# Kernel tuning notes

Measured on AMD Instinct MI355X. Metric: run time of the kernel, lower is better.

## Reference

```python
import jax, jax.numpy as jnp
import numpy as np

D_MODEL = 1024
NUM_HEADS = 16
HEAD_DIM = D_MODEL // NUM_HEADS
B, S = 2, 2048
EPS = 1e-8


def setup_inputs() -> dict:
    key = jax.random.key(0)
    ks = jax.random.split(key, 9)
    sc = 1.0 / np.sqrt(D_MODEL)
    return {
        "x": jax.random.normal(ks[0], (B, S, D_MODEL), jnp.float32),
        "wq": jax.random.normal(ks[1], (D_MODEL, D_MODEL), jnp.float32) * sc,
        "bq": jax.random.normal(ks[2], (D_MODEL,), jnp.float32) * 0.01,
        "wk": jax.random.normal(ks[3], (D_MODEL, D_MODEL), jnp.float32) * sc,
        "bk": jax.random.normal(ks[4], (D_MODEL,), jnp.float32) * 0.01,
        "wv": jax.random.normal(ks[5], (D_MODEL, D_MODEL), jnp.float32) * sc,
        "bv": jax.random.normal(ks[6], (D_MODEL,), jnp.float32) * 0.01,
        "wo": jax.random.normal(ks[7], (D_MODEL, D_MODEL), jnp.float32) * sc,
        "bo": jax.random.normal(ks[8], (D_MODEL,), jnp.float32) * 0.01,
    }


def reference(x, wq, bq, wk, bk, wv, bv, wo, bo):
    b, s, d = x.shape
    h, hd = NUM_HEADS, HEAD_DIM
    # projections (torch Linear: y = x W^T + b); reshape to [b, h, s, hd]
    def proj(w, bias):
        return (jnp.einsum('bsd,ed->bse', x, w) + bias).reshape(b, s, h, hd).transpose(0, 2, 1, 3)
    q = proj(wq, bq)
    k = proj(wk, bk)
    v = proj(wv, bv)
    scores = jnp.einsum('bhqd,bhkd->bhqk', q, k) / np.sqrt(hd)
    attn = jax.nn.softmax(scores, axis=-1)
    o = jnp.einsum('bhqk,bhkd->bhqd', attn, v)  # [b, h, s, hd]
    # per-position, per-head Gram-Schmidt exclusion: remove component of o[i]
    # along v[i] (the loop in the original is independent over positions)
    v_norm_sq = jnp.sum(v * v, axis=-1, keepdims=True)          # [b,h,s,1]
    align = jnp.sum(o * v, axis=-1, keepdims=True) / (v_norm_sq + EPS)
    o = o - align * v
    o = o.transpose(0, 2, 1, 3).reshape(b, s, d)
    return jnp.einsum('bsd,ed->bse', o, wo) + bo
```

## Files before the change

### kernel.cpp

```cpp
#include <hip/hip_runtime.h>
#include <stdint.h>

#define SEQ 2048
#define NTOK 4096
#define DM 1024

typedef __bf16 bf16x8 __attribute__((ext_vector_type(8)));
typedef __bf16 bf16x4 __attribute__((ext_vector_type(4)));
typedef float f32x4 __attribute__((ext_vector_type(4)));

__device__ __forceinline__ unsigned short f2bf(float f) {
  union { float f; unsigned u; } v; v.f = f;
  return (unsigned short)((v.u + 0x7fffu + ((v.u >> 16) & 1u)) >> 16);
}
__device__ __forceinline__ float bf2f(unsigned short s) {
  union { unsigned u; float f; } v; v.u = ((unsigned)s) << 16; return v.f;
}
__device__ __forceinline__ unsigned pkbf(float a, float b) {
  union { float f; unsigned u; } x, y; x.f = a; y.f = b;
  return __builtin_amdgcn_perm(y.u + 0x8000u, x.u + 0x8000u, 0x07060302u);
}

__device__ __forceinline__ void async16(const unsigned short* g, unsigned short* l) {
  __builtin_amdgcn_global_load_lds(
      (const __attribute__((address_space(1))) void*)g,
      (__attribute__((address_space(3))) void*)l, 16, 0, 0);
}

__global__ __launch_bounds__(256) void cast_all(
    const float* __restrict__ x, const float* __restrict__ wq,
    const float* __restrict__ wk, const float* __restrict__ wv,
    const float* __restrict__ wo, unsigned short* __restrict__ dst) {
  size_t i = ((size_t)blockIdx.x * 256 + threadIdx.x) * 4;
  const float* src; size_t off;
  if (i < (size_t)NTOK * DM) { src = x; off = i; }
  else {
    size_t j = i - (size_t)NTOK * DM;
    int s = (int)(j >> 20);
    src = (s == 0) ? wq : (s == 1) ? wk : (s == 2) ? wv : wo;
    off = j & 1048575u;
  }
  float4 f = *(const float4*)(src + off);
  ushort4 o;
  o.x = f2bf(f.x); o.y = f2bf(f.y); o.z = f2bf(f.z); o.w = f2bf(f.w);
  *(ushort4*)(dst + i) = o;
}

__device__ __forceinline__ void gemm128_bk64(
    const unsigned short* __restrict__ A, const unsigned short* __restrict__ Bw,
    int m0, int n0, f32x4 acc[4][4], unsigned short* As, unsigned short* Bs) {
  const int tid = threadIdx.x, lane = tid & 63, w = tid >> 6;
  const int wm = (w >> 1) * 64, wn = (w & 1) * 64;
  const int quad = lane >> 4, l16 = lane & 15, sel = l16 & 7;
  const int srow = tid >> 3;
  const int sc = ((tid & 7) ^ (srow & 7)) << 3;

  for (int kt = 0; kt < 1024; kt += 64) {
    __syncthreads();
#pragma unroll
    for (int c = 0; c < 4; ++c) {
      const int row = c * 32 + srow;
      async16(A + (size_t)(m0 + row) * 1024 + kt + sc, As + c * 2048 + tid * 8);
      async16(Bw + (size_t)(n0 + row) * 1024 + kt + sc, Bs + c * 2048 + tid * 8);
    }
    __syncthreads();
#pragma unroll
    for (int ks = 0; ks < 2; ++ks) {
      bf16x8 af[4], bf[4];
#pragma unroll
      for (int i = 0; i < 4; ++i)
        af[i] = *(const bf16x8*)(As + (wm + i * 16 + l16) * 64 + (((ks * 4 + quad) ^ sel) << 3));
#pragma unroll
      for (int j = 0; j < 4; ++j)
        bf[j] = *(const bf16x8*)(Bs + (wn + j * 16 + l16) * 64 + (((ks * 4 + quad) ^ sel) << 3));
#pragma unroll
      for (int i = 0; i < 4; ++i)
#pragma unroll
        for (int j = 0; j < 4; ++j)
          acc[i][j] = __builtin_amdgcn_mfma_f32_16x16x32_bf16(af[i], bf[j], acc[i][j], 0, 0, 0);
    }
  }
}

__global__ __launch_bounds__(256) void qkv_gemm(
    const unsigned short* __restrict__ xb,
    const unsigned short* __restrict__ wqb, const unsigned short* __restrict__ wkb,
    const unsigned short* __restrict__ wvb,
    const float* __restrict__ bq, const float* __restrict__ bk, const float* __restrict__ bv,
    unsigned short* __restrict__ Q, unsigned short* __restrict__ Kd,
    unsigned short* __restrict__ Vt) {
  __shared__ unsigned short As[128 * 64], Bs[128 * 64];
  const int kind = blockIdx.z;
  const unsigned short* A; const unsigned short* Bw;
  int m0, n0;
  if (kind == 2) { A = wvb; Bw = xb; m0 = blockIdx.x * 128; n0 = blockIdx.y * 128; }
  else { A = xb; Bw = (kind == 0) ? wqb : wkb; m0 = blockIdx.y * 128; n0 = blockIdx.x * 128; }
  f32x4 acc[4][4];
#pragma unroll
  for (int i = 0; i < 4; ++i)
#pragma unroll
    for (int j = 0; j < 4; ++j) { f32x4 z = {0.f, 0.f, 0.f, 0.f}; acc[i][j] = z; }
  gemm128_bk64(A, Bw, m0, n0, acc, As, Bs);

  const int lane = threadIdx.x & 63, w = threadIdx.x >> 6;
  const int quad = lane >> 4, l16 = lane & 15;
  const int wm = (w >> 1) * 64, wn = (w & 1) * 64;

  if (kind == 2) {
#pragma unroll
    for (int i = 0; i < 4; ++i)
#pragma unroll
      for (int j = 0; j < 4; ++j) {
        const int n = n0 + wn + j * 16 + l16;
        const int tb = n >> 11, s = n & 2047;
#pragma unroll
        for (int r = 0; r < 4; ++r) {
          const int m = m0 + wm + i * 16 + quad * 4 + r;
          const int h = m >> 6, d = m & 63;
          Vt[((size_t)(tb * 16 + h) * 64 + d) * SEQ + s] = f2bf(acc[i][j][r] + bv[m]);
        }
      }
  } else {
    const float* bias = (kind == 0) ? bq : bk;
    const float scale = (kind == 0) ? 0.180336880f : 1.0f;
#pragma unroll
    for (int i = 0; i < 4; ++i)
#pragma unroll
      for (int j = 0; j < 4; ++j) {
        const int col = n0 + wn + j * 16 + l16;
        const float bb = bias[col];
        const int h = col >> 6, d = col & 63;
#pragma unroll
        for (int r = 0; r < 4; ++r) {
          const int m = m0 + wm + i * 16 + quad * 4 + r;
          const int b = m >> 11, s = m & 2047;
          const int bh = b * 16 + h;
          const unsigned short val = f2bf((acc[i][j][r] + bb) * scale);
          if (kind == 0) Q[((size_t)bh * SEQ + s) * 64 + d] = val;
          else           Kd[((size_t)bh * SEQ + s) * 64 + d] = val;
        }
      }
  }
}

__global__ __launch_bounds__(256, 2) void attn_kernel(
    const unsigned short* __restrict__ Q, const unsigned short* __restrict__ Kd,
    const unsigned short* __restrict__ Vt,
    unsigned short* __restrict__ Op, float* __restrict__ Lp) {
  __shared__ unsigned short KV[4][4096];
  const int gx = blockIdx.x;
  const int xcd = gx & 7;
  const int idx = gx >> 3;
  const int bh  = xcd * 4 + (idx & 3);
  const int ksl = (idx >> 2) & 1;
  const int q0  = (idx >> 3) * 256;
  const int ks0 = ksl << 10;
  const int tid = threadIdx.x, lane = tid & 63, w = tid >> 6;
  const int quad = lane >> 4, l16 = lane & 15;
  const unsigned short* Qp = Q + (size_t)bh * SEQ * 64;
  const unsigned short* Kp = Kd + (size_t)bh * SEQ * 64;
  const unsigned short* Vp = Vt + (size_t)bh * 64 * SEQ;
  const int srow = tid >> 3;
  const int sc = ((tid & 7) ^ (srow & 7)) << 3;

#pragma unroll
  for (int c = 0; c < 8; ++c)
    async16(Qp + (size_t)(q0 + c * 32 + srow) * 64 + sc,
            KV[c >> 1] + (c & 1) * 2048 + tid * 8);
  __syncthreads();

  const int sel = l16 & 7;
  const unsigned short* Qsrc = KV[w];
  bf16x8 bQ[4][2];
#pragma unroll
  for (int qq = 0; qq < 4; ++qq) {
    const int qrow = qq * 16 + l16;
#pragma unroll
    for (int hh = 0; hh < 2; ++hh)
      bQ[qq][hh] = *(const bf16x8*)(Qsrc + qrow * 64 + (((hh * 4 + quad) ^ sel) << 3));
  }
  __syncthreads();

  async16(Kp + (size_t)(ks0 + srow) * 64 + sc, KV[0] + tid * 8);
  async16(Kp + (size_t)(ks0 + 32 + srow) * 64 + sc, KV[0] + 2048 + tid * 8);
  async16(Vp + (size_t)srow * SEQ + ks0 + sc, KV[2] + tid * 8);
  async16(Vp + (size_t)(32 + srow) * SEQ + ks0 + sc, KV[2] + 2048 + tid * 8);

  union { unsigned short u[8]; bf16x8 v; } one8;
#pragma unroll
  for (int t = 0; t < 8; ++t) one8.u[t] = 0x3F80;
  const bf16x8 aOnes = one8.v;

  f32x4 o_acc[4][4];
  f32x4 l_acc[4];
  const f32x4 zinit = {-12.f, -12.f, -12.f, -12.f};
#pragma unroll
  for (int qq = 0; qq < 4; ++qq) {
    f32x4 z = {0.f, 0.f, 0.f, 0.f};
    l_acc[qq] = z;
#pragma unroll
    for (int dt = 0; dt < 4; ++dt) o_acc[qq][dt] = z;
  }

  for (int it = 0; it < 16; ++it) {
    const int cur = it & 1;
    __syncthreads();
    if (it + 1 < 16) {
      const int kt = ks0 + (it + 1) * 64, nb = (it + 1) & 1;
      async16(Kp + (size_t)(kt + srow) * 64 + sc, KV[nb] + tid * 8);
      async16(Kp + (size_t)(kt + 32 + srow) * 64 + sc, KV[nb] + 2048 + tid * 8);
      async16(Vp + (size_t)srow * SEQ + kt + sc, KV[2 + nb] + tid * 8);
      async16(Vp + (size_t)(32 + srow) * SEQ + kt + sc, KV[2 + nb] + 2048 + tid * 8);
    }
    const unsigned short* Ks = KV[cur];
    const unsigned short* Vs = KV[2 + cur];

    bf16x8 bP[4][2];
#pragma unroll
    for (int kk = 0; kk < 4; ++kk) {
      const int krow = kk * 16 + l16;
      bf16x8 a0 = *(const bf16x8*)(Ks + krow * 64 + ((quad ^ sel) << 3));
      bf16x8 a1 = *(const bf16x8*)(Ks + krow * 64 + (((4 + quad) ^ sel) << 3));
#pragma unroll
      for (int qq = 0; qq < 4; ++qq) {
        f32x4 z = __builtin_amdgcn_mfma_f32_16x16x32_bf16(a0, bQ[qq][0], zinit, 0, 0, 0);
        z = __builtin_amdgcn_mfma_f32_16x16x32_bf16(a1, bQ[qq][1], z, 0, 0, 0);
#pragma unroll
        for (int r = 0; r < 4; ++r) z[r] = __builtin_amdgcn_exp2f(z[r]);
        unsigned lo = pkbf(z[0], z[1]);
        unsigned hi = pkbf(z[2], z[3]);
        union { unsigned d[4]; bf16x8 v; } pk;
        pk.v = bP[qq][kk >> 1];
        pk.d[(kk & 1) * 2] = lo;
        pk.d[(kk & 1) * 2 + 1] = hi;
        bP[qq][kk >> 1] = pk.v;
      }
    }

#pragma unroll
    for (int qq = 0; qq < 4; ++qq)
#pragma unroll
      for (int G = 0; G < 2; ++G)
        l_acc[qq] = __builtin_amdgcn_mfma_f32_16x16x32_bf16(aOnes, bP[qq][G], l_acc[qq], 0, 0, 0);

#pragma unroll
    for (int dt = 0; dt < 4; ++dt) {
      const unsigned short* vbase = Vs + (dt * 16 + l16) * 64;
      const int inner = (quad & 1) * 4;
#pragma unroll
      for (int G = 0; G < 2; ++G) {
        const int c0 = 4 * G + (quad >> 1);
        bf16x4 lo = *(const bf16x4*)(vbase + ((c0 ^ sel) << 3) + inner);
        bf16x4 hi = *(const bf16x4*)(vbase + (((c0 + 2) ^ sel) << 3) + inner);
        bf16x8 aV = __builtin_shufflevector(lo, hi, 0, 1, 2, 3, 4, 5, 6, 7);
#pragma unroll
        for (int qq = 0; qq < 4; ++qq)
          o_acc[qq][dt] = __builtin_amdgcn_mfma_f32_16x16x32_bf16(aV, bP[qq][G], o_acc[qq][dt], 0, 0, 0);
      }
    }
  }

  const size_t sb = (size_t)(ksl * 32 + bh);
#pragma unroll
  for (int qq = 0; qq < 4; ++qq) {
    const int qg = q0 + w * 64 + qq * 16 + l16;
#pragma unroll
    for (int dt = 0; dt < 4; ++dt)
#pragma unroll
      for (int r = 0; r < 4; ++r) {
        const int d = dt * 16 + quad * 4 + r;
        Op[(sb * 64 + d) * SEQ + qg] = f2bf(o_acc[qq][dt][r]);
      }
    if (quad == 0) Lp[sb * SEQ + qg] = l_acc[qq][0];
  }
}

__global__ __launch_bounds__(128) void combine_kernel(
    const unsigned short* __restrict__ Op, const float* __restrict__ Lp,
    const unsigned short* __restrict__ Vt, unsigned short* __restrict__ O) {
  const int bh = blockIdx.y;
  const int q = blockIdx.x * 128 + threadIdx.x;
  const size_t QC = (size_t)32 * SEQ;
  const size_t idx = (size_t)bh * SEQ + q;
  const float inv = 1.0f / (Lp[idx] + Lp[QC + idx]);
  const unsigned short* O1 = Op + (size_t)bh * 64 * SEQ + q;
  const unsigned short* O2 = O1 + QC * 64;
  const unsigned short* Vp = Vt + (size_t)bh * 64 * SEQ + q;
  float o64[64];
  float ov = 0.f, vv = 0.f;
#pragma unroll
  for (int d = 0; d < 64; ++d) {
    const float o = (bf2f(O1[(size_t)d * SEQ]) + bf2f(O2[(size_t)d * SEQ])) * inv;
    const float v = bf2f(Vp[(size_t)d * SEQ]);
    o64[d] = o; ov += o * v; vv += v * v;
  }
  const float align = ov / (vv + 1e-8f);
  const int b = bh >> 4, h = bh & 15;
  unsigned short* dst = O + (size_t)(b * SEQ + q) * DM + h * 64;
#pragma unroll
  for (int d = 0; d < 64; d += 2) {
    const float a0 = o64[d]     - align * bf2f(Vp[(size_t)d * SEQ]);
    const float a1 = o64[d + 1] - align * bf2f(Vp[(size_t)(d + 1) * SEQ]);
    *(unsigned*)(dst + d) = pkbf(a0, a1);
  }
}

__global__ __launch_bounds__(256) void out_gemm(
    const unsigned short* __restrict__ Ob, const unsigned short* __restrict__ wob,
    const float* __restrict__ bo, float* __restrict__ out) {
  __shared__ unsigned short As[64 * 64], Bs[128 * 64];
  const int m0 = blockIdx.y * 64, n0 = blockIdx.x * 128;
  const int tid = threadIdx.x, lane = tid & 63, w = tid >> 6;
  const int wm = (w >> 1) * 32, wn = (w & 1) * 64;
  const int quad = lane >> 4, l16 = lane & 15, sel = l16 & 7;
  const int srow = tid >> 3;
  const int sc = ((tid & 7) ^ (srow & 7)) << 3;
  f32x4 acc[2][4];
#pragma unroll
  for (int i = 0; i < 2; ++i)
#pragma unroll
    for (int j = 0; j < 4; ++j) { f32x4 z = {0.f, 0.f, 0.f, 0.f}; acc[i][j] = z; }

  for (int kt = 0; kt < 1024; kt += 64) {
    __syncthreads();
#pragma unroll
    for (int c = 0; c < 2; ++c) {
      const int row = c * 32 + srow;
      async16(Ob + (size_t)(m0 + row) * 1024 + kt + sc, As + c * 2048 + tid * 8);
    }
#pragma unroll
    for (int c = 0; c < 4; ++c) {
      const int row = c * 32 + srow;
      async16(wob + (size_t)(n0 + row) * 1024 + kt + sc, Bs + c * 2048 + tid * 8);
    }
    __syncthreads();
#pragma unroll
    for (int ks = 0; ks < 2; ++ks) {
      bf16x8 af[2], bf[4];
#pragma unroll
      for (int i = 0; i < 2; ++i)
        af[i] = *(const bf16x8*)(As + (wm + i * 16 + l16) * 64 + (((ks * 4 + quad) ^ sel) << 3));
#pragma unroll
      for (int j = 0; j < 4; ++j)
        bf[j] = *(const bf16x8*)(Bs + (wn + j * 16 + l16) * 64 + (((ks * 4 + quad) ^ sel) << 3));
#pragma unroll
      for (int i = 0; i < 2; ++i)
#pragma unroll
        for (int j = 0; j < 4; ++j)
          acc[i][j] = __builtin_amdgcn_mfma_f32_16x16x32_bf16(af[i], bf[j], acc[i][j], 0, 0, 0);
    }
  }

#pragma unroll
  for (int i = 0; i < 2; ++i)
#pragma unroll
    for (int j = 0; j < 4; ++j) {
      const int col = n0 + wn + j * 16 + l16;
      const float bb = bo[col];
#pragma unroll
      for (int r = 0; r < 4; ++r) {
        const int m = m0 + wm + i * 16 + quad * 4 + r;
        out[(size_t)m * DM + col] = acc[i][j][r] + bb;
      }
    }
}

extern "C" void kernel_launch(void* const* d_in, const int* in_sizes, int n_in,
                              void* d_out, int out_size, void* d_ws, size_t ws_size,
                              hipStream_t stream) {
  const float* x  = (const float*)d_in[0];
  const float* wq = (const float*)d_in[1];
  const float* bq = (const float*)d_in[2];
  const float* wk = (const float*)d_in[3];
  const float* bk = (const float*)d_in[4];
  const float* wv = (const float*)d_in[5];
  const float* bv = (const float*)d_in[6];
  const float* wo = (const float*)d_in[7];
  const float* bo = (const float*)d_in[8];
  float* out = (float*)d_out;
  (void)in_sizes; (void)n_in; (void)out_size; (void)ws_size;

  unsigned short* ws  = (unsigned short*)d_ws;
  unsigned short* xb  = ws;
  unsigned short* wqb = xb + (size_t)NTOK * DM;
  unsigned short* wkb = wqb + (size_t)DM * DM;
  unsigned short* wvb = wkb + (size_t)DM * DM;
  unsigned short* wob = wvb + (size_t)DM * DM;
  unsigned short* Qb  = wob + (size_t)DM * DM;
  unsigned short* Kb  = Qb + (size_t)NTOK * DM;
  unsigned short* Vtb = Kb + (size_t)NTOK * DM;
  unsigned short* Ob  = Vtb + (size_t)NTOK * DM;
  unsigned short* Opb = Ob + (size_t)NTOK * DM;
  float* Lpw = (float*)(Opb + (size_t)2 * 32 * 64 * SEQ);

  cast_all<<<8192, 256, 0, stream>>>(x, wq, wk, wv, wo, ws);
  qkv_gemm<<<dim3(8, 32, 3), 256, 0, stream>>>(xb, wqb, wkb, wvb, bq, bk, bv, Qb, Kb, Vtb);
  attn_kernel<<<512, 256, 0, stream>>>(Qb, Kb, Vtb, Opb, Lpw);
  combine_kernel<<<dim3(16, 32), 128, 0, stream>>>(Opb, Lpw, Vtb, Ob);
  out_gemm<<<dim3(8, 64), 256, 0, stream>>>(Ob, wob, bo, out);
}
```

Baseline: 197.1 us.

## Double-buffer LDS in QKV and output GEMMs and remap QKV block order

Both projection GEMMs now use two 32-wide K buffers in shared memory. The next tile is issued asynchronously before the current tile's MFMAs, which removes one barrier per iteration and overlaps global-to-LDS loads with compute. The QKV launch becomes a flat 1D grid, with block indices remapped so blocks that share token tiles are grouped together for better L2 reuse. Halving BK doubles the number of loop iterations and barriers, and the swizzle is reworked for the 32-wide rows.

Measured after the change: 210.3 us. +6.7%, slower.

```diff
diff --git a/kernel.cpp b/kernel.cpp
--- a/kernel.cpp
+++ b/kernel.cpp
@@ -46,42 +46,6 @@
   *(ushort4*)(dst + i) = o;
 }
 
-__device__ __forceinline__ void gemm128_bk64(
-    const unsigned short* __restrict__ A, const unsigned short* __restrict__ Bw,
-    int m0, int n0, f32x4 acc[4][4], unsigned short* As, unsigned short* Bs) {
-  const int tid = threadIdx.x, lane = tid & 63, w = tid >> 6;
-  const int wm = (w >> 1) * 64, wn = (w & 1) * 64;
-  const int quad = lane >> 4, l16 = lane & 15, sel = l16 & 7;
-  const int srow = tid >> 3;
-  const int sc = ((tid & 7) ^ (srow & 7)) << 3;
-
-  for (int kt = 0; kt < 1024; kt += 64) {
-    __syncthreads();
-#pragma unroll
-    for (int c = 0; c < 4; ++c) {
-      const int row = c * 32 + srow;
-      async16(A + (size_t)(m0 + row) * 1024 + kt + sc, As + c * 2048 + tid * 8);
-      async16(Bw + (size_t)(n0 + row) * 1024 + kt + sc, Bs + c * 2048 + tid * 8);
-    }
-    __syncthreads();
-#pragma unroll
-    for (int ks = 0; ks < 2; ++ks) {
-      bf16x8 af[4], bf[4];
-#pragma unroll
-      for (int i = 0; i < 4; ++i)
-        af[i] = *(const bf16x8*)(As + (wm + i * 16 + l16) * 64 + (((ks * 4 + quad) ^ sel) << 3));
-#pragma unroll
-      for (int j = 0; j < 4; ++j)
-        bf[j] = *(const bf16x8*)(Bs + (wn + j * 16 + l16) * 64 + (((ks * 4 + quad) ^ sel) << 3));
-#pragma unroll
-      for (int i = 0; i < 4; ++i)
-#pragma unroll
-        for (int j = 0; j < 4; ++j)
-          acc[i][j] = __builtin_amdgcn_mfma_f32_16x16x32_bf16(af[i], bf[j], acc[i][j], 0, 0, 0);
-    }
-  }
-}
-
 __global__ __launch_bounds__(256) void qkv_gemm(
     const unsigned short* __restrict__ xb,
     const unsigned short* __restrict__ wqb, const unsigned short* __restrict__ wkb,
@@ -89,22 +53,61 @@
     const float* __restrict__ bq, const float* __restrict__ bk, const float* __restrict__ bv,
     unsigned short* __restrict__ Q, unsigned short* __restrict__ Kd,
     unsigned short* __restrict__ Vt) {
-  __shared__ unsigned short As[128 * 64], Bs[128 * 64];
-  const int kind = blockIdx.z;
+  __shared__ unsigned short As[2][128 * 32], Bs[2][128 * 32];
+  const int gx = blockIdx.x;
+  const int kind = gx >> 8;
+  const int rr = gx & 255;
+  const int tok = 4 * (rr & 7) + ((rr >> 3) & 3);
+  const int oth = rr >> 5;
   const unsigned short* A; const unsigned short* Bw;
   int m0, n0;
-  if (kind == 2) { A = wvb; Bw = xb; m0 = blockIdx.x * 128; n0 = blockIdx.y * 128; }
-  else { A = xb; Bw = (kind == 0) ? wqb : wkb; m0 = blockIdx.y * 128; n0 = blockIdx.x * 128; }
+  if (kind == 2) { A = wvb; Bw = xb; m0 = oth * 128; n0 = tok * 128; }
+  else { A = xb; Bw = kind ? wkb : wqb; m0 = tok * 128; n0 = oth * 128; }
+
+  const int tid = threadIdx.x, lane = tid & 63, w = tid >> 6;
+  const int wm = (w >> 1) * 64, wn = (w & 1) * 64;
+  const int quad = lane >> 4, l16 = lane & 15;
+  const int srow = tid >> 2;
+  const int sc = (((tid & 3) ^ (srow & 3)) << 3);
+
   f32x4 acc[4][4];
 #pragma unroll
   for (int i = 0; i < 4; ++i)
 #pragma unroll
     for (int j = 0; j < 4; ++j) { f32x4 z = {0.f, 0.f, 0.f, 0.f}; acc[i][j] = z; }
-  gemm128_bk64(A, Bw, m0, n0, acc, As, Bs);
-
-  const int lane = threadIdx.x & 63, w = threadIdx.x >> 6;
-  const int quad = lane >> 4, l16 = lane & 15;
-  const int wm = (w >> 1) * 64, wn = (w & 1) * 64;
+
+  async16(A + (size_t)(m0 + srow) * 1024 + sc, As[0] + tid * 8);
+  async16(A + (size_t)(m0 + 64 + srow) * 1024 + sc, As[0] + 2048 + tid * 8);
+  async16(Bw + (size_t)(n0 + srow) * 1024 + sc, Bs[0] + tid * 8);
+  async16(Bw + (size_t)(n0 + 64 + srow) * 1024 + sc, Bs[0] + 2048 + tid * 8);
+
+  for (int it = 0; it < 32; ++it) {
+    const int cur = it & 1;
+    __syncthreads();
+    if (it + 1 < 32) {
+      const int kt = (it + 1) * 32, nb = (it + 1) & 1;
+      async16(A + (size_t)(m0 + srow) * 1024 + kt + sc, As[nb] + tid * 8);
+      async16(A + (size_t)(m0 + 64 + srow) * 1024 + kt + sc, As[nb] + 2048 + tid * 8);
+      async16(Bw + (size_t)(n0 + srow) * 1024 + kt + sc, Bs[nb] + tid * 8);
+      async16(Bw + (size_t)(n0 + 64 + srow) * 1024 + kt + sc, Bs[nb] + 2048 + tid * 8);
+    }
+    bf16x8 af[4], bf[4];
+#pragma unroll
+    for (int i = 0; i < 4; ++i) {
+      const int r = wm + i * 16 + l16;
+      af[i] = *(const bf16x8*)(As[cur] + r * 32 + ((quad ^ (r & 3)) << 3));
+    }
+#pragma unroll
+    for (int j = 0; j < 4; ++j) {
+      const int r = wn + j * 16 + l16;
+      bf[j] = *(const bf16x8*)(Bs[cur] + r * 32 + ((quad ^ (r & 3)) << 3));
+    }
+#pragma unroll
+    for (int i = 0; i < 4; ++i)
+#pragma unroll
+      for (int j = 0; j < 4; ++j)
+        acc[i][j] = __builtin_amdgcn_mfma_f32_16x16x32_bf16(af[i], bf[j], acc[i][j], 0, 0, 0);
+  }
 
   if (kind == 2) {
 #pragma unroll
@@ -308,47 +311,48 @@
 __global__ __launch_bounds__(256) void out_gemm(
     const unsigned short* __restrict__ Ob, const unsigned short* __restrict__ wob,
     const float* __restrict__ bo, float* __restrict__ out) {
-  __shared__ unsigned short As[64 * 64], Bs[128 * 64];
+  __shared__ unsigned short As[2][64 * 32], Bs[2][128 * 32];
   const int m0 = blockIdx.y * 64, n0 = blockIdx.x * 128;
   const int tid = threadIdx.x, lane = tid & 63, w = tid >> 6;
   const int wm = (w >> 1) * 32, wn = (w & 1) * 64;
-  const int quad = lane >> 4, l16 = lane & 15, sel = l16 & 7;
-  const int srow = tid >> 3;
-  const int sc = ((tid & 7) ^ (srow & 7)) << 3;
+  const int quad = lane >> 4, l16 = lane & 15;
+  const int srow = tid >> 2;
+  const int sc = (((tid & 3) ^ (srow & 3)) << 3);
   f32x4 acc[2][4];
 #pragma unroll
   for (int i = 0; i < 2; ++i)
 #pragma unroll
     for (int j = 0; j < 4; ++j) { f32x4 z = {0.f, 0.f, 0.f, 0.f}; acc[i][j] = z; }
 
-  for (int kt = 0; kt < 1024; kt += 64) {
+  async16(Ob + (size_t)(m0 + srow) * 1024 + sc, As[0] + tid * 8);
+  async16(wob + (size_t)(n0 + srow) * 1024 + sc, Bs[0] + tid * 8);
+  async16(wob + (size_t)(n0 + 64 + srow) * 1024 + sc, Bs[0] + 2048 + tid * 8);
+
+  for (int it = 0; it < 32; ++it) {
+    const int cur = it & 1;
     __syncthreads();
-#pragma unroll
-    for (int c = 0; c < 2; ++c) {
-      const int row = c * 32 + srow;
-      async16(Ob + (size_t)(m0 + row) * 1024 + kt + sc, As + c * 2048 + tid * 8);
-    }
-#pragma unroll
-    for (int c = 0; c < 4; ++c) {
-      const int row = c * 32 + srow;
-      async16(wob + (size_t)(n0 + row) * 1024 + kt + sc, Bs + c * 2048 + tid * 8);
-    }
-    __syncthreads();
-#pragma unroll
-    for (int ks = 0; ks < 2; ++ks) {
-      bf16x8 af[2], bf[4];
-#pragma unroll
-      for (int i = 0; i < 2; ++i)
-        af[i] = *(const bf16x8*)(As + (wm + i * 16 + l16) * 64 + (((ks * 4 + quad) ^ sel) << 3));
+    if (it + 1 < 32) {
+      const int kt = (it + 1) * 32, nb = (it + 1) & 1;
+      async16(Ob + (size_t)(m0 + srow) * 1024 + kt + sc, As[nb] + tid * 8);
+      async16(wob + (size_t)(n0 + srow) * 1024 + kt + sc, Bs[nb] + tid * 8);
+      async16(wob + (size_t)(n0 + 64 + srow) * 1024 + kt + sc, Bs[nb] + 2048 + tid * 8);
+    }
+    bf16x8 af[2], bf[4];
+#pragma unroll
+    for (int i = 0; i < 2; ++i) {
+      const int r = wm + i * 16 + l16;
+      af[i] = *(const bf16x8*)(As[cur] + r * 32 + ((quad ^ (r & 3)) << 3));
+    }
+#pragma unroll
+    for (int j = 0; j < 4; ++j) {
+      const int r = wn + j * 16 + l16;
+      bf[j] = *(const bf16x8*)(Bs[cur] + r * 32 + ((quad ^ (r & 3)) << 3));
+    }
+#pragma unroll
+    for (int i = 0; i < 2; ++i)
 #pragma unroll
       for (int j = 0; j < 4; ++j)
-        bf[j] = *(const bf16x8*)(Bs + (wn + j * 16 + l16) * 64 + (((ks * 4 + quad) ^ sel) << 3));
-#pragma unroll
-      for (int i = 0; i < 2; ++i)
-#pragma unroll
-        for (int j = 0; j < 4; ++j)
-          acc[i][j] = __builtin_amdgcn_mfma_f32_16x16x32_bf16(af[i], bf[j], acc[i][j], 0, 0, 0);
-    }
+        acc[i][j] = __builtin_amdgcn_mfma_f32_16x16x32_bf16(af[i], bf[j], acc[i][j], 0, 0, 0);
   }
 
 #pragma unroll
@@ -394,7 +398,7 @@
   float* Lpw = (float*)(Opb + (size_t)2 * 32 * 64 * SEQ);
 
   cast_all<<<8192, 256, 0, stream>>>(x, wq, wk, wv, wo, ws);
-  qkv_gemm<<<dim3(8, 32, 3), 256, 0, stream>>>(xb, wqb, wkb, wvb, bq, bk, bv, Qb, Kb, Vtb);
+  qkv_gemm<<<768, 256, 0, stream>>>(xb, wqb, wkb, wvb, bq, bk, bv, Qb, Kb, Vtb);
   attn_kernel<<<512, 256, 0, stream>>>(Qb, Kb, Vtb, Opb, Lpw);
   combine_kernel<<<dim3(16, 32), 128, 0, stream>>>(Opb, Lpw, Vtb, Ob);
   out_gemm<<<dim3(8, 64), 256, 0, stream>>>(Ob, wob, bo, out);
```
